# Performance work log

Measured on AMD Instinct MI355X. Metric: run time of the kernel, lower is better.

## Reference

```python
import jax, jax.numpy as jnp
import numpy as np

N = 50000      # nodes
E = 800000     # edges (before self-loops)
IN = 128       # in_channels
C = 64         # hidden_channels (per head)
H = 2          # heads
OUT = 40       # out_channels (classes)
SLOPE = 0.2    # PyG GATConv leaky_relu negative_slope


def setup_inputs() -> dict:
    key = jax.random.key(0)
    ks = jax.random.split(key, 12)
    def glorot(k, shape, fan):
        return (jax.random.normal(k, shape, jnp.float32) / np.float32(np.sqrt(fan)))
    x = jax.random.normal(ks[0], (N, IN), jnp.float32)
    edge_index = jax.random.randint(ks[1], (2, E), 0, N, dtype=jnp.int32)
    return {
        "x": x,
        "edge_index": edge_index,
        "W0": glorot(ks[2], (IN, H * C), IN),
        "a_src0": glorot(ks[3], (H, C), C),
        "a_dst0": glorot(ks[4], (H, C), C),
        "b0": jnp.zeros((H * C,), jnp.float32),
        "W1": glorot(ks[5], (H * C, H * C), H * C),
        "a_src1": glorot(ks[6], (H, C), C),
        "a_dst1": glorot(ks[7], (H, C), C),
        "b1": jnp.zeros((H * C,), jnp.float32),
        "lin_w": glorot(ks[8], (H * C * 2, OUT), H * C * 2),
        "lin_b": jnp.zeros((OUT,), jnp.float32),
    }


def gat_conv(x, W, a_src, a_dst, b, src, dst):
    # x: [N, F_in] -> h: [N, H, C]
    h = (x @ W).reshape(-1, H, C)
    # per-node attention logits (PyG splits a into src/dst halves)
    es = jnp.einsum("nhc,hc->nh", h, a_src)  # [N, H]
    ed = jnp.einsum("nhc,hc->nh", h, a_dst)  # [N, H]
    e = jax.nn.leaky_relu(es[src] + ed[dst], SLOPE)  # [Etot, H]
    # segment softmax over incoming edges of each destination node
    m = jax.ops.segment_max(e, dst, num_segments=N)          # [N, H]
    m = jnp.where(jnp.isneginf(m), 0.0, m)
    w = jnp.exp(e - m[dst])                                  # [Etot, H]
    denom = jax.ops.segment_sum(w, dst, num_segments=N)      # [N, H]
    alpha = w / jnp.maximum(denom[dst], 1e-16)               # [Etot, H]
    # scatter-aggregate messages: [Etot, H, C] -> [N, H, C]
    out = jax.ops.segment_sum(alpha[:, :, None] * h[src], dst, num_segments=N)
    return out.reshape(-1, H * C) + b  # concat=True over heads


def reference(x, edge_index, W0, a_src0, a_dst0, b0, W1, a_src1, a_dst1, b1, lin_w, lin_b):
    # PyG GATConv adds self-loops by default
    loops = jnp.arange(N, dtype=edge_index.dtype)
    src = jnp.concatenate([edge_index[0], loops])
    dst = jnp.concatenate([edge_index[1], loops])
    h1 = jax.nn.elu(gat_conv(x, W0, a_src0, a_dst0, b0, src, dst))   # [N, H*C]
    h2 = jax.nn.elu(gat_conv(h1, W1, a_src1, a_dst1, b1, src, dst))  # [N, H*C]
    h_cat = jnp.concatenate([h1, h2], axis=1)                        # [N, 2*H*C]
    logits = h_cat @ lin_w + lin_b                                   # [N, OUT]
    return jax.nn.log_softmax(logits, axis=1)
```

## Files before the change

### kernel.cpp

```cpp
#include <hip/hip_runtime.h>
#include <hip/hip_fp16.h>
#include <math.h>

#define NN 50000
#define E0 800000
#define ET 850000
#define NBK 196
#define TILE 4096
#define NTILES 208
#define CAP 8192

typedef unsigned int uint32;
typedef unsigned short u16;
typedef __attribute__((ext_vector_type(8))) _Float16 f16x8;
typedef __attribute__((ext_vector_type(4))) float f32x4;

__device__ __forceinline__ u16 f2h(float f) {
  return __half_as_ushort(__float2half(f));
}
__device__ __forceinline__ float h2f(u16 u) {
  return __half2float(__ushort_as_half(u));
}

__global__ __launch_bounds__(256) void partition_prep_kernel(
    const int* __restrict__ ei, int* __restrict__ gcursor, uint32* __restrict__ packed,
    const float* __restrict__ W0, const float* __restrict__ W1,
    const float* __restrict__ lw,
    u16* __restrict__ w0t, u16* __restrict__ w1t, u16* __restrict__ lwt)
{
  __shared__ __align__(16) char smem[23872];
  const int b = blockIdx.x;
  const int tid = threadIdx.x;
  if (b < NTILES) {
    int* hist = (int*)smem;
    int* s    = (int*)(smem + 784);
    int* scanb = (int*)(smem + 1808);
    int* gofs  = (int*)(smem + 2592);
    uint32* shuf = (uint32*)(smem + 3376);
    unsigned char* sbkt = (unsigned char*)(smem + 19760);
    const int t0 = b * TILE;
    for (int i = tid; i < NBK; i += 256) hist[i] = 0;
    __syncthreads();
    int myb[16]; int myr[16]; uint32 mypk[16];
#pragma unroll
    for (int it = 0; it < 4; ++it) {
      const int q = it * 256 + tid;
      const int e4 = t0 + q * 4;
      const bool valid = (e4 < ET);
      int sa[4], da[4];
      if (valid) {
        if (e4 + 3 < E0) {
          int4 sv = *(const int4*)&ei[e4];
          int4 dv = *(const int4*)&ei[E0 + e4];
          sa[0] = sv.x; sa[1] = sv.y; sa[2] = sv.z; sa[3] = sv.w;
          da[0] = dv.x; da[1] = dv.y; da[2] = dv.z; da[3] = dv.w;
        } else {
#pragma unroll
          for (int u = 0; u < 4; ++u) { sa[u] = e4 - E0 + u; da[u] = sa[u]; }
        }
      }
#pragma unroll
      for (int u = 0; u < 4; ++u) {
        const int i = it * 4 + u;
        myb[i] = -1;
        if (valid) {
          const int src = sa[u], dst = da[u];
          myb[i] = dst >> 8;
          mypk[i] = ((uint32)(dst & 255) << 16) | (uint32)src;
          myr[i] = atomicAdd(&hist[myb[i]], 1);
        }
      }
    }
    __syncthreads();
    int v = (tid < NBK) ? hist[tid] : 0;
    int val = v;
    s[tid] = val;
    __syncthreads();
#pragma unroll
    for (int off = 1; off < 256; off <<= 1) {
      int t = (tid >= off) ? s[tid - off] : 0;
      __syncthreads();
      val += t;
      s[tid] = val;
      __syncthreads();
    }
    if (tid < NBK) {
      scanb[tid] = val - v;
      gofs[tid] = (v > 0) ? atomicAdd(&gcursor[tid], v) : 0;
    }
    __syncthreads();
#pragma unroll
    for (int i = 0; i < 16; ++i) {
      if (myb[i] >= 0) {
        int slot = scanb[myb[i]] + myr[i];
        shuf[slot] = mypk[i];
        sbkt[slot] = (unsigned char)myb[i];
      }
    }
    __syncthreads();
    const int tcount = (t0 + TILE <= ET) ? TILE : (ET - t0);
    for (int i = tid; i < tcount; i += 256) {
      int bb = sbkt[i];
      packed[(size_t)bb * CAP + gofs[bb] + (i - scanb[bb])] = shuf[i];
    }
  } else if (b < NTILES + 2) {
    const float* W = (b == NTILES) ? W0 : W1;
    u16* Wt = (b == NTILES) ? w0t : w1t;
    float (*tile)[129] = (float(*)[129])smem;
    for (int k0 = 0; k0 < 128; k0 += 32) {
      __syncthreads();
#pragma unroll
      for (int it = 0; it < 4; ++it) {
        int q = tid + it * 256;
        int kk = q >> 5, n4 = (q & 31) * 4;
        float4 v = *(const float4*)&W[(k0 + kk) * 128 + n4];
        tile[kk][n4 + 0] = v.x; tile[kk][n4 + 1] = v.y;
        tile[kk][n4 + 2] = v.z; tile[kk][n4 + 3] = v.w;
      }
      __syncthreads();
      int n = tid >> 1, h = (tid & 1) * 16;
      __align__(16) u16 tmp[16];
#pragma unroll
      for (int j = 0; j < 16; ++j) tmp[j] = f2h(tile[h + j][n]);
      *(uint4*)&Wt[n * 128 + k0 + h] = *(uint4*)&tmp[0];
      *(uint4*)&Wt[n * 128 + k0 + h + 8] = *(uint4*)&tmp[8];
    }
  } else {
    for (int idx = tid; idx < 48 * 256; idx += 256) {
      int j = idx >> 8, k = idx & 255;
      lwt[idx] = (j < 40) ? f2h(lw[k * 40 + j]) : (u16)0;
    }
  }
}

__device__ __forceinline__ void build_body(
    char* smem, int b,
    const uint32* __restrict__ packed, const int* __restrict__ gcursor,
    int2* __restrict__ rowinfo, u16* __restrict__ csr_src)
{
  int* h      = (int*)smem;
  int* s      = (int*)(smem + 1024);
  int* sc     = (int*)(smem + 2048);
  int* cur    = (int*)(smem + 3072);
  int* ptot_p = (int*)(smem + 4096);
  u16* simg   = (u16*)(smem + 4112);
  const int tid = threadIdx.x;
  const int cnt = gcursor[b];
  const uint32* pk = packed + (size_t)b * CAP;
  h[tid] = 0;
  cur[tid] = 0;
  __syncthreads();
  for (int i = tid; i < cnt; i += 256) atomicAdd(&h[(pk[i] >> 16) & 255], 1);
  __syncthreads();
  const int pd = (h[tid] + 7) & ~7;
  int val = pd;
  s[tid] = val;
  __syncthreads();
#pragma unroll
  for (int off = 1; off < 256; off <<= 1) {
    int t = (tid >= off) ? s[tid - off] : 0;
    __syncthreads();
    val += t;
    s[tid] = val;
    __syncthreads();
  }
  sc[tid] = val - pd;
  if (tid == 255) *ptot_p = val;
  __syncthreads();
  const int ptot = *ptot_p;
  for (int i = tid; i < ptot; i += 256) simg[i] = (u16)NN;
  __syncthreads();
  for (int i = tid; i < cnt; i += 256) {
    uint32 p = pk[i];
    int dl = (p >> 16) & 255;
    int r = atomicAdd(&cur[dl], 1);
    simg[sc[dl] + r] = (u16)(p & 0xFFFFu);
  }
  __syncthreads();
  int n = b * 256 + tid;
  if (n < NN) rowinfo[n] = make_int2(b * CAP + sc[tid], pd);
  uint32* dst = (uint32*)(csr_src + (size_t)b * CAP);
  const uint32* sim32 = (const uint32*)simg;
  for (int i = tid; i < (ptot >> 1); i += 256) dst[i] = sim32[i];
}

__global__ __launch_bounds__(256) void gemm_att_kernel(
    const float* __restrict__ Xf, const u16* __restrict__ Xh,
    const u16* __restrict__ Wt,
    const float* __restrict__ avs, const float* __restrict__ avd,
    u16* __restrict__ hfeat, float* __restrict__ es, float* __restrict__ ed,
    int nnodes,
    const uint32* __restrict__ packed, const int* __restrict__ gcursor,
    int2* __restrict__ rowinfo, u16* __restrict__ csr_src)
{
  __shared__ __align__(16) char smem[20608];
  const int ngemm = (nnodes + 63) >> 6;
  if ((int)blockIdx.x >= ngemm) {
    build_body(smem, (int)blockIdx.x - ngemm, packed, gcursor, rowinfo, csr_src);
    return;
  }
  u16* hout   = (u16*)smem;
  float* es_s = (float*)(smem + 17408);
  float* ed_s = (float*)(smem + 17920);
  const int tid = threadIdx.x;
  const int wid = tid >> 6, lane = tid & 63;
  const int quad = lane >> 4, lc = lane & 15;
  const int n0 = blockIdx.x * 64;
  if (blockIdx.x == 0 && tid < 2) es[2 * NN + tid] = -1e30f;

  const int arow = wid * 16 + lc;
  const int rrow = min(n0 + arow, nnodes - 1);

  f32x4 acc[8];
#pragma unroll
  for (int t = 0; t < 8; ++t) acc[t] = (f32x4){0.f, 0.f, 0.f, 0.f};
#pragma unroll
  for (int ks = 0; ks < 4; ++ks) {
    const int k0 = ks * 32 + quad * 8;
    f16x8 a;
    if (Xf) {
      const float4* xr = (const float4*)&Xf[(size_t)rrow * 128 + k0];
      float4 v0 = xr[0], v1 = xr[1];
      a[0] = (_Float16)v0.x; a[1] = (_Float16)v0.y;
      a[2] = (_Float16)v0.z; a[3] = (_Float16)v0.w;
      a[4] = (_Float16)v1.x; a[5] = (_Float16)v1.y;
      a[6] = (_Float16)v1.z; a[7] = (_Float16)v1.w;
    } else {
      a = *(const f16x8*)&Xh[(size_t)rrow * 128 + k0];
    }
#pragma unroll
    for (int t = 0; t < 8; ++t) {
      f16x8 bfr = *(const f16x8*)&Wt[(t * 16 + lc) * 128 + k0];
      acc[t] = __builtin_amdgcn_mfma_f32_16x16x32_f16(a, bfr, acc[t], 0, 0, 0);
    }
  }

  float av_s[8], av_d[8];
#pragma unroll
  for (int t = 0; t < 8; ++t) { av_s[t] = avs[t * 16 + lc]; av_d[t] = avd[t * 16 + lc]; }
#pragma unroll
  for (int r = 0; r < 4; ++r) {
    float s0 = 0.f, s1 = 0.f, d0 = 0.f, d1 = 0.f;
#pragma unroll
    for (int t = 0; t < 4; ++t) { s0 += acc[t][r] * av_s[t]; d0 += acc[t][r] * av_d[t]; }
#pragma unroll
    for (int t = 4; t < 8; ++t) { s1 += acc[t][r] * av_s[t]; d1 += acc[t][r] * av_d[t]; }
#pragma unroll
    for (int m = 1; m < 16; m <<= 1) {
      s0 += __shfl_xor(s0, m); s1 += __shfl_xor(s1, m);
      d0 += __shfl_xor(d0, m); d1 += __shfl_xor(d1, m);
    }
    if (lc == 0) {
      int row = wid * 16 + quad * 4 + r;
      es_s[row] = s0; es_s[64 + row] = s1;
      ed_s[row] = d0; ed_s[64 + row] = d1;
    }
  }
#pragma unroll
  for (int t = 0; t < 8; ++t)
#pragma unroll
    for (int r = 0; r < 4; ++r)
      hout[(wid * 16 + quad * 4 + r) * 136 + t * 16 + lc] = f2h(acc[t][r]);
  __syncthreads();
#pragma unroll
  for (int it = 0; it < 4; ++it) {
    int g = tid + it * 256;
    int r = g >> 4, c8 = (g & 15) * 8;
    if (n0 + r < nnodes)
      *(uint4*)&hfeat[(size_t)(n0 + r) * 128 + c8] = *(const uint4*)&hout[r * 136 + c8];
  }
  if (tid < 64) {
    int n = n0 + tid;
    if (n < nnodes) {
      es[n * 2 + 0] = es_s[tid];      es[n * 2 + 1] = es_s[64 + tid];
      ed[n * 2 + 0] = ed_s[tid];      ed[n * 2 + 1] = ed_s[64 + tid];
    }
  }
}

__global__ __launch_bounds__(256) void aggregate_kernel(
    const uint4* __restrict__ hfeat4, const float* __restrict__ es, const float* __restrict__ ed,
    const int2* __restrict__ rowinfo, const u16* __restrict__ csr_src,
    const float* __restrict__ bias, u16* __restrict__ out, int nnodes)
{
  int n = (blockIdx.x * blockDim.x + threadIdx.x) >> 6;
  int lane = threadIdx.x & 63;
  if (n >= nnodes) return;
  const int eg = lane >> 4;
  const int fl = lane & 15;
  const int hd = (fl >= 8) ? 1 : 0;
  const int2 ri = rowinfo[n];
  const int nch = ri.y >> 3;
  const int j0 = ri.x + eg;
  const float edn = ed[n * 2 + hd];

  float acc[8];
#pragma unroll
  for (int t = 0; t < 8; ++t) acc[t] = 0.f;
  float den = 0.f;

  int iA0 = csr_src[j0], iA1 = csr_src[j0 + 4];
  float e0 = es[iA0 * 2 + hd] + edn; e0 = fmaxf(e0, 0.2f * e0);
  float e1 = es[iA1 * 2 + hd] + edn; e1 = fmaxf(e1, 0.2f * e1);
  float wA0 = __expf(e0), wA1 = __expf(e1);
  uint4 hA0 = hfeat4[(size_t)iA0 * 16 + fl];
  uint4 hA1 = hfeat4[(size_t)iA1 * 16 + fl];

  for (int c = 0;;) {
    const bool more = (c + 1 < nch);
    float wB0 = 0.f, wB1 = 0.f; uint4 hB0, hB1;
    if (more) {
      const int jb = j0 + (c + 1) * 8;
      int iB0 = csr_src[jb], iB1 = csr_src[jb + 4];
      float f0 = es[iB0 * 2 + hd] + edn; f0 = fmaxf(f0, 0.2f * f0);
      float f1 = es[iB1 * 2 + hd] + edn; f1 = fmaxf(f1, 0.2f * f1);
      wB0 = __expf(f0); wB1 = __expf(f1);
      hB0 = hfeat4[(size_t)iB0 * 16 + fl];
      hB1 = hfeat4[(size_t)iB1 * 16 + fl];
    }
    acc[0] = fmaf(wA0, h2f((u16)(hA0.x & 0xFFFFu)), acc[0]);
    acc[1] = fmaf(wA0, h2f((u16)(hA0.x >> 16)),     acc[1]);
    acc[2] = fmaf(wA0, h2f((u16)(hA0.y & 0xFFFFu)), acc[2]);
    acc[3] = fmaf(wA0, h2f((u16)(hA0.y >> 16)),     acc[3]);
    acc[4] = fmaf(wA0, h2f((u16)(hA0.z & 0xFFFFu)), acc[4]);
    acc[5] = fmaf(wA0, h2f((u16)(hA0.z >> 16)),     acc[5]);
    acc[6] = fmaf(wA0, h2f((u16)(hA0.w & 0xFFFFu)), acc[6]);
    acc[7] = fmaf(wA0, h2f((u16)(hA0.w >> 16)),     acc[7]);
    acc[0] = fmaf(wA1, h2f((u16)(hA1.x & 0xFFFFu)), acc[0]);
    acc[1] = fmaf(wA1, h2f((u16)(hA1.x >> 16)),     acc[1]);
    acc[2] = fmaf(wA1, h2f((u16)(hA1.y & 0xFFFFu)), acc[2]);
    acc[3] = fmaf(wA1, h2f((u16)(hA1.y >> 16)),     acc[3]);
    acc[4] = fmaf(wA1, h2f((u16)(hA1.z & 0xFFFFu)), acc[4]);
    acc[5] = fmaf(wA1, h2f((u16)(hA1.z >> 16)),     acc[5]);
    acc[6] = fmaf(wA1, h2f((u16)(hA1.w & 0xFFFFu)), acc[6]);
    acc[7] = fmaf(wA1, h2f((u16)(hA1.w >> 16)),     acc[7]);
    den += wA0 + wA1;
    if (!more) break;
    wA0 = wB0; wA1 = wB1; hA0 = hB0; hA1 = hB1;
    ++c;
  }

#pragma unroll
  for (int t = 0; t < 8; ++t) {
    acc[t] += __shfl_xor(acc[t], 16);
    acc[t] += __shfl_xor(acc[t], 32);
  }
  den += __shfl_xor(den, 16);
  den += __shfl_xor(den, 32);

  if (eg == 0) {
    float inv = 1.f / den;
    float4 b0 = *(const float4*)&bias[fl * 8];
    float4 b1 = *(const float4*)&bias[fl * 8 + 4];
    float bv[8] = {b0.x, b0.y, b0.z, b0.w, b1.x, b1.y, b1.z, b1.w};
    u16 pk[8];
#pragma unroll
    for (int t = 0; t < 8; ++t) {
      float v = acc[t] * inv + bv[t];
      v = (v > 0.f) ? v : (__expf(v) - 1.f);
      pk[t] = f2h(v);
    }
    uint4 o;
    o.x = (uint32)pk[0] | ((uint32)pk[1] << 16);
    o.y = (uint32)pk[2] | ((uint32)pk[3] << 16);
    o.z = (uint32)pk[4] | ((uint32)pk[5] << 16);
    o.w = (uint32)pk[6] | ((uint32)pk[7] << 16);
    ((uint4*)out)[(size_t)n * 16 + fl] = o;
  }
}

__global__ __launch_bounds__(256) void final_kernel(
    const u16* __restrict__ h1b, const u16* __restrict__ h2b,
    const u16* __restrict__ lwt, const float* __restrict__ lb,
    float* __restrict__ out, int nnodes)
{
  const int tid = threadIdx.x;
  const int wid = tid >> 6, lane = tid & 63;
  const int quad = lane >> 4, lc = lane & 15;
  const int n0 = blockIdx.x * 64;
  const int arow = wid * 16 + lc;
  const int rrow = min(n0 + arow, nnodes - 1);

  f32x4 acc[3];
#pragma unroll
  for (int t = 0; t < 3; ++t) acc[t] = (f32x4){0.f, 0.f, 0.f, 0.f};
#pragma unroll
  for (int ks = 0; ks < 8; ++ks) {
    const u16* hsrc = (ks < 4) ? h1b : h2b;
    const int k0 = (ks & 3) * 32 + quad * 8;
    const int kl = ks * 32 + quad * 8;
    f16x8 a = *(const f16x8*)&hsrc[(size_t)rrow * 128 + k0];
#pragma unroll
    for (int t = 0; t < 3; ++t) {
      f16x8 b = *(const f16x8*)&lwt[(t * 16 + lc) * 256 + kl];
      acc[t] = __builtin_amdgcn_mfma_f32_16x16x32_f16(a, b, acc[t], 0, 0, 0);
    }
  }

  float bv[3];
  bool valid[3];
#pragma unroll
  for (int t = 0; t < 3; ++t) {
    int col = t * 16 + lc;
    valid[t] = (col < 40);
    bv[t] = valid[t] ? lb[col] : 0.f;
  }
#pragma unroll
  for (int r = 0; r < 4; ++r) {
    int row = wid * 16 + quad * 4 + r;
    int n = n0 + row;
    float v[3];
    float mx = -INFINITY;
#pragma unroll
    for (int t = 0; t < 3; ++t) {
      v[t] = acc[t][r] + bv[t];
      if (valid[t]) mx = fmaxf(mx, v[t]);
    }
    mx = fmaxf(mx, __shfl_xor(mx, 1));
    mx = fmaxf(mx, __shfl_xor(mx, 2));
    mx = fmaxf(mx, __shfl_xor(mx, 4));
    mx = fmaxf(mx, __shfl_xor(mx, 8));
    float s = 0.f;
#pragma unroll
    for (int t = 0; t < 3; ++t) if (valid[t]) s += __expf(v[t] - mx);
    s += __shfl_xor(s, 1);
    s += __shfl_xor(s, 2);
    s += __shfl_xor(s, 4);
    s += __shfl_xor(s, 8);
    float lg = mx + __logf(s);
    if (n < nnodes) {
#pragma unroll
      for (int t = 0; t < 3; ++t)
        if (valid[t]) out[(size_t)n * 40 + t * 16 + lc] = v[t] - lg;
    }
  }
}


extern "C" void kernel_launch(void* const* d_in, const int* in_sizes, int n_in,
                              void* d_out, int out_size, void* d_ws, size_t ws_size,
                              hipStream_t stream) {
  const float* x   = (const float*)d_in[0];
  const int*   ei  = (const int*)d_in[1];
  const float* W0  = (const float*)d_in[2];
  const float* as0 = (const float*)d_in[3];
  const float* ad0 = (const float*)d_in[4];
  const float* b0  = (const float*)d_in[5];
  const float* W1  = (const float*)d_in[6];
  const float* as1 = (const float*)d_in[7];
  const float* ad1 = (const float*)d_in[8];
  const float* b1  = (const float*)d_in[9];
  const float* lw  = (const float*)d_in[10];
  const float* lb  = (const float*)d_in[11];
  float* out = (float*)d_out;

  char* p = (char*)d_ws;
  auto carve = [&](size_t bytes) { char* r = p; p += (bytes + 255) & ~(size_t)255; return r; };
  u16* w0t    = (u16*)carve(128 * 128 * 2);
  u16* w1t    = (u16*)carve(128 * 128 * 2);
  u16* lwt    = (u16*)carve(48 * 256 * 2);
  u16* hfeat  = (u16*)carve((size_t)(NN + 1) * 128 * 2);
  u16* h1b    = (u16*)carve((size_t)NN * 128 * 2);
  u16* h2b    = (u16*)carve((size_t)NN * 128 * 2);
  float* es   = (float*)carve((size_t)(NN + 1) * 2 * 4);
  float* ed   = (float*)carve((size_t)NN * 2 * 4);
  int2* rowinfo = (int2*)carve((size_t)NN * 8);
  u16* csr    = (u16*)carve((size_t)NBK * CAP * 2);
  uint32* packed = (uint32*)carve((size_t)NBK * CAP * 4);
  int* gcursor = (int*)carve(NBK * 4);

  hipMemsetAsync(gcursor, 0, NBK * 4, stream);

  const int NG = (NN + 63) / 64;

  partition_prep_kernel<<<NTILES + 3, 256, 0, stream>>>(
      ei, gcursor, packed, W0, W1, lw, w0t, w1t, lwt);

  gemm_att_kernel<<<NG + NBK, 256, 0, stream>>>(
      x, nullptr, w0t, as0, ad0, hfeat, es, ed, NN, packed, gcursor, rowinfo, csr);
  aggregate_kernel<<<(NN * 64 + 255) / 256, 256, 0, stream>>>(
      (const uint4*)hfeat, es, ed, rowinfo, csr, b0, h1b, NN);

  gemm_att_kernel<<<NG, 256, 0, stream>>>(
      nullptr, h1b, w1t, as1, ad1, hfeat, es, ed, NN, packed, gcursor, rowinfo, csr);
  aggregate_kernel<<<(NN * 64 + 255) / 256, 256, 0, stream>>>(
      (const uint4*)hfeat, es, ed, rowinfo, csr, b1, h2b, NN);

  final_kernel<<<NG, 256, 0, stream>>>(h1b, h2b, lwt, lb, out, NN);
}
```

Before: 234.6 us.

## Halve partition tile size, use wave-shuffle block scan, make aggregation grid-stride

Partition tiles shrink from 4096 to 2048 edges, doubling the tile block count and cutting shared memory per block. The Hillis-Steele shared-memory scans in the partition and CSR-build bodies become a wave shuffle scan plus a 4-wave fixup, removing most barriers. The aggregate kernel becomes a persistent grid-stride loop over nodes with 2048 blocks and the bias loaded once per wave. Risks include more global atomics on the bucket cursors and load imbalance in the fixed-grid aggregation.

Result: no change. 238.7 us (+1.8%).

```diff
diff --git a/kernel.cpp b/kernel.cpp
--- a/kernel.cpp
+++ b/kernel.cpp
@@ -6,8 +6,8 @@
 #define E0 800000
 #define ET 850000
 #define NBK 196
-#define TILE 4096
-#define NTILES 208
+#define TILE 2048
+#define NTILES 416
 #define CAP 8192
 
 typedef unsigned int uint32;
@@ -20,6 +20,22 @@
 }
 __device__ __forceinline__ float h2f(u16 u) {
   return __half2float(__ushort_as_half(u));
+}
+
+__device__ __forceinline__ int block_incl_scan(int v, int tid, int* wsum) {
+  const int lane = tid & 63, wid = tid >> 6;
+  int val = v;
+#pragma unroll
+  for (int off = 1; off < 64; off <<= 1) {
+    int t = __shfl_up(val, off);
+    if (lane >= off) val += t;
+  }
+  if (lane == 63) wsum[wid] = val;
+  __syncthreads();
+  int wofs = 0;
+#pragma unroll
+  for (int w = 0; w < 4; ++w) wofs += (w < wid) ? wsum[w] : 0;
+  return val + wofs;
 }
 
 __global__ __launch_bounds__(256) void partition_prep_kernel(
@@ -28,22 +44,22 @@
     const float* __restrict__ lw,
     u16* __restrict__ w0t, u16* __restrict__ w1t, u16* __restrict__ lwt)
 {
-  __shared__ __align__(16) char smem[23872];
+  __shared__ __align__(16) char smem[16512];
   const int b = blockIdx.x;
   const int tid = threadIdx.x;
   if (b < NTILES) {
-    int* hist = (int*)smem;
-    int* s    = (int*)(smem + 784);
-    int* scanb = (int*)(smem + 1808);
-    int* gofs  = (int*)(smem + 2592);
-    uint32* shuf = (uint32*)(smem + 3376);
-    unsigned char* sbkt = (unsigned char*)(smem + 19760);
+    int* hist  = (int*)smem;
+    int* scanb = (int*)(smem + 1024);
+    int* gofs  = (int*)(smem + 2048);
+    int* wsum  = (int*)(smem + 3072);
+    uint32* shuf = (uint32*)(smem + 3088);
+    unsigned char* sbkt = (unsigned char*)(smem + 11280);
     const int t0 = b * TILE;
-    for (int i = tid; i < NBK; i += 256) hist[i] = 0;
+    hist[tid] = 0;
     __syncthreads();
-    int myb[16]; int myr[16]; uint32 mypk[16];
-#pragma unroll
-    for (int it = 0; it < 4; ++it) {
+    int myb[8]; int myr[8]; uint32 mypk[8];
+#pragma unroll
+    for (int it = 0; it < 2; ++it) {
       const int q = it * 256 + tid;
       const int e4 = t0 + q * 4;
       const bool valid = (e4 < ET);
@@ -72,25 +88,15 @@
       }
     }
     __syncthreads();
-    int v = (tid < NBK) ? hist[tid] : 0;
-    int val = v;
-    s[tid] = val;
+    const int v = (tid < NBK) ? hist[tid] : 0;
+    const int incl = block_incl_scan(v, tid, wsum);
+    if (tid < NBK) {
+      scanb[tid] = incl - v;
+      gofs[tid] = (v > 0) ? atomicAdd(&gcursor[tid], v) : 0;
+    }
     __syncthreads();
 #pragma unroll
-    for (int off = 1; off < 256; off <<= 1) {
-      int t = (tid >= off) ? s[tid - off] : 0;
-      __syncthreads();
-      val += t;
-      s[tid] = val;
-      __syncthreads();
-    }
-    if (tid < NBK) {
-      scanb[tid] = val - v;
-      gofs[tid] = (v > 0) ? atomicAdd(&gcursor[tid], v) : 0;
-    }
-    __syncthreads();
-#pragma unroll
-    for (int i = 0; i < 16; ++i) {
+    for (int i = 0; i < 8; ++i) {
       if (myb[i] >= 0) {
         int slot = scanb[myb[i]] + myr[i];
         shuf[slot] = mypk[i];
@@ -139,11 +145,11 @@
     int2* __restrict__ rowinfo, u16* __restrict__ csr_src)
 {
   int* h      = (int*)smem;
-  int* s      = (int*)(smem + 1024);
-  int* sc     = (int*)(smem + 2048);
-  int* cur    = (int*)(smem + 3072);
-  int* ptot_p = (int*)(smem + 4096);
-  u16* simg   = (u16*)(smem + 4112);
+  int* sc     = (int*)(smem + 1024);
+  int* cur    = (int*)(smem + 2048);
+  int* wsum   = (int*)(smem + 3072);
+  int* ptot_p = (int*)(smem + 3088);
+  u16* simg   = (u16*)(smem + 3104);
   const int tid = threadIdx.x;
   const int cnt = gcursor[b];
   const uint32* pk = packed + (size_t)b * CAP;
@@ -153,19 +159,9 @@
   for (int i = tid; i < cnt; i += 256) atomicAdd(&h[(pk[i] >> 16) & 255], 1);
   __syncthreads();
   const int pd = (h[tid] + 7) & ~7;
-  int val = pd;
-  s[tid] = val;
-  __syncthreads();
-#pragma unroll
-  for (int off = 1; off < 256; off <<= 1) {
-    int t = (tid >= off) ? s[tid - off] : 0;
-    __syncthreads();
-    val += t;
-    s[tid] = val;
-    __syncthreads();
-  }
-  sc[tid] = val - pd;
-  if (tid == 255) *ptot_p = val;
+  const int incl = block_incl_scan(pd, tid, wsum);
+  sc[tid] = incl - pd;
+  if (tid == 255) *ptot_p = incl;
   __syncthreads();
   const int ptot = *ptot_p;
   for (int i = tid; i < ptot; i += 256) simg[i] = (u16)NN;
@@ -283,89 +279,97 @@
     const int2* __restrict__ rowinfo, const u16* __restrict__ csr_src,
     const float* __restrict__ bias, u16* __restrict__ out, int nnodes)
 {
-  int n = (blockIdx.x * blockDim.x + threadIdx.x) >> 6;
-  int lane = threadIdx.x & 63;
-  if (n >= nnodes) return;
+  const int wgid = (blockIdx.x * blockDim.x + threadIdx.x) >> 6;
+  const int nwaves = (gridDim.x * blockDim.x) >> 6;
+  const int lane = threadIdx.x & 63;
   const int eg = lane >> 4;
   const int fl = lane & 15;
   const int hd = (fl >= 8) ? 1 : 0;
-  const int2 ri = rowinfo[n];
-  const int nch = ri.y >> 3;
-  const int j0 = ri.x + eg;
-  const float edn = ed[n * 2 + hd];
-
-  float acc[8];
-#pragma unroll
-  for (int t = 0; t < 8; ++t) acc[t] = 0.f;
-  float den = 0.f;
-
-  int iA0 = csr_src[j0], iA1 = csr_src[j0 + 4];
-  float e0 = es[iA0 * 2 + hd] + edn; e0 = fmaxf(e0, 0.2f * e0);
-  float e1 = es[iA1 * 2 + hd] + edn; e1 = fmaxf(e1, 0.2f * e1);
-  float wA0 = __expf(e0), wA1 = __expf(e1);
-  uint4 hA0 = hfeat4[(size_t)iA0 * 16 + fl];
-  uint4 hA1 = hfeat4[(size_t)iA1 * 16 + fl];
-
-  for (int c = 0;;) {
-    const bool more = (c + 1 < nch);
-    float wB0 = 0.f, wB1 = 0.f; uint4 hB0, hB1;
-    if (more) {
-      const int jb = j0 + (c + 1) * 8;
-      int iB0 = csr_src[jb], iB1 = csr_src[jb + 4];
-      float f0 = es[iB0 * 2 + hd] + edn; f0 = fmaxf(f0, 0.2f * f0);
-      float f1 = es[iB1 * 2 + hd] + edn; f1 = fmaxf(f1, 0.2f * f1);
-      wB0 = __expf(f0); wB1 = __expf(f1);
-      hB0 = hfeat4[(size_t)iB0 * 16 + fl];
-      hB1 = hfeat4[(size_t)iB1 * 16 + fl];
-    }
-    acc[0] = fmaf(wA0, h2f((u16)(hA0.x & 0xFFFFu)), acc[0]);
-    acc[1] = fmaf(wA0, h2f((u16)(hA0.x >> 16)),     acc[1]);
-    acc[2] = fmaf(wA0, h2f((u16)(hA0.y & 0xFFFFu)), acc[2]);
-    acc[3] = fmaf(wA0, h2f((u16)(hA0.y >> 16)),     acc[3]);
-    acc[4] = fmaf(wA0, h2f((u16)(hA0.z & 0xFFFFu)), acc[4]);
-    acc[5] = fmaf(wA0, h2f((u16)(hA0.z >> 16)),     acc[5]);
-    acc[6] = fmaf(wA0, h2f((u16)(hA0.w & 0xFFFFu)), acc[6]);
-    acc[7] = fmaf(wA0, h2f((u16)(hA0.w >> 16)),     acc[7]);
-    acc[0] = fmaf(wA1, h2f((u16)(hA1.x & 0xFFFFu)), acc[0]);
-    acc[1] = fmaf(wA1, h2f((u16)(hA1.x >> 16)),     acc[1]);
-    acc[2] = fmaf(wA1, h2f((u16)(hA1.y & 0xFFFFu)), acc[2]);
-    acc[3] = fmaf(wA1, h2f((u16)(hA1.y >> 16)),     acc[3]);
-    acc[4] = fmaf(wA1, h2f((u16)(hA1.z & 0xFFFFu)), acc[4]);
-    acc[5] = fmaf(wA1, h2f((u16)(hA1.z >> 16)),     acc[5]);
-    acc[6] = fmaf(wA1, h2f((u16)(hA1.w & 0xFFFFu)), acc[6]);
-    acc[7] = fmaf(wA1, h2f((u16)(hA1.w >> 16)),     acc[7]);
-    den += wA0 + wA1;
-    if (!more) break;
-    wA0 = wB0; wA1 = wB1; hA0 = hB0; hA1 = hB1;
-    ++c;
-  }
-
-#pragma unroll
-  for (int t = 0; t < 8; ++t) {
-    acc[t] += __shfl_xor(acc[t], 16);
-    acc[t] += __shfl_xor(acc[t], 32);
-  }
-  den += __shfl_xor(den, 16);
-  den += __shfl_xor(den, 32);
-
-  if (eg == 0) {
-    float inv = 1.f / den;
+
+  float bv[8];
+  {
     float4 b0 = *(const float4*)&bias[fl * 8];
     float4 b1 = *(const float4*)&bias[fl * 8 + 4];
-    float bv[8] = {b0.x, b0.y, b0.z, b0.w, b1.x, b1.y, b1.z, b1.w};
-    u16 pk[8];
+    bv[0] = b0.x; bv[1] = b0.y; bv[2] = b0.z; bv[3] = b0.w;
+    bv[4] = b1.x; bv[5] = b1.y; bv[6] = b1.z; bv[7] = b1.w;
+  }
+
+  for (int n = wgid; n < nnodes; n += nwaves) {
+    const int2 ri = rowinfo[n];
+    const int nch = ri.y >> 3;
+    const int j0 = ri.x + eg;
+    const float edn = ed[n * 2 + hd];
+
+    float acc[8];
+#pragma unroll
+    for (int t = 0; t < 8; ++t) acc[t] = 0.f;
+    float den = 0.f;
+
+    int iA0 = csr_src[j0], iA1 = csr_src[j0 + 4];
+    float e0 = es[iA0 * 2 + hd] + edn; e0 = fmaxf(e0, 0.2f * e0);
+    float e1 = es[iA1 * 2 + hd] + edn; e1 = fmaxf(e1, 0.2f * e1);
+    float wA0 = __expf(e0), wA1 = __expf(e1);
+    uint4 hA0 = hfeat4[(size_t)iA0 * 16 + fl];
+    uint4 hA1 = hfeat4[(size_t)iA1 * 16 + fl];
+
+    for (int c = 0;;) {
+      const bool more = (c + 1 < nch);
+      float wB0 = 0.f, wB1 = 0.f; uint4 hB0, hB1;
+      if (more) {
+        const int jb = j0 + (c + 1) * 8;
+        int iB0 = csr_src[jb], iB1 = csr_src[jb + 4];
+        float f0 = es[iB0 * 2 + hd] + edn; f0 = fmaxf(f0, 0.2f * f0);
+        float f1 = es[iB1 * 2 + hd] + edn; f1 = fmaxf(f1, 0.2f * f1);
+        wB0 = __expf(f0); wB1 = __expf(f1);
+        hB0 = hfeat4[(size_t)iB0 * 16 + fl];
+        hB1 = hfeat4[(size_t)iB1 * 16 + fl];
+      }
+      acc[0] = fmaf(wA0, h2f((u16)(hA0.x & 0xFFFFu)), acc[0]);
+      acc[1] = fmaf(wA0, h2f((u16)(hA0.x >> 16)),     acc[1]);
+      acc[2] = fmaf(wA0, h2f((u16)(hA0.y & 0xFFFFu)), acc[2]);
+      acc[3] = fmaf(wA0, h2f((u16)(hA0.y >> 16)),     acc[3]);
+      acc[4] = fmaf(wA0, h2f((u16)(hA0.z & 0xFFFFu)), acc[4]);
+      acc[5] = fmaf(wA0, h2f((u16)(hA0.z >> 16)),     acc[5]);
+      acc[6] = fmaf(wA0, h2f((u16)(hA0.w & 0xFFFFu)), acc[6]);
+      acc[7] = fmaf(wA0, h2f((u16)(hA0.w >> 16)),     acc[7]);
+      acc[0] = fmaf(wA1, h2f((u16)(hA1.x & 0xFFFFu)), acc[0]);
+      acc[1] = fmaf(wA1, h2f((u16)(hA1.x >> 16)),     acc[1]);
+      acc[2] = fmaf(wA1, h2f((u16)(hA1.y & 0xFFFFu)), acc[2]);
+      acc[3] = fmaf(wA1, h2f((u16)(hA1.y >> 16)),     acc[3]);
+      acc[4] = fmaf(wA1, h2f((u16)(hA1.z & 0xFFFFu)), acc[4]);
+      acc[5] = fmaf(wA1, h2f((u16)(hA1.z >> 16)),     acc[5]);
+      acc[6] = fmaf(wA1, h2f((u16)(hA1.w & 0xFFFFu)), acc[6]);
+      acc[7] = fmaf(wA1, h2f((u16)(hA1.w >> 16)),     acc[7]);
+      den += wA0 + wA1;
+      if (!more) break;
+      wA0 = wB0; wA1 = wB1; hA0 = hB0; hA1 = hB1;
+      ++c;
+    }
+
 #pragma unroll
     for (int t = 0; t < 8; ++t) {
-      float v = acc[t] * inv + bv[t];
-      v = (v > 0.f) ? v : (__expf(v) - 1.f);
-      pk[t] = f2h(v);
-    }
-    uint4 o;
-    o.x = (uint32)pk[0] | ((uint32)pk[1] << 16);
-    o.y = (uint32)pk[2] | ((uint32)pk[3] << 16);
-    o.z = (uint32)pk[4] | ((uint32)pk[5] << 16);
-    o.w = (uint32)pk[6] | ((uint32)pk[7] << 16);
-    ((uint4*)out)[(size_t)n * 16 + fl] = o;
+      acc[t] += __shfl_xor(acc[t], 16);
+      acc[t] += __shfl_xor(acc[t], 32);
+    }
+    den += __shfl_xor(den, 16);
+    den += __shfl_xor(den, 32);
+
+    if (eg == 0) {
+      float inv = 1.f / den;
+      u16 pk[8];
+#pragma unroll
+      for (int t = 0; t < 8; ++t) {
+        float v = acc[t] * inv + bv[t];
+        v = (v > 0.f) ? v : (__expf(v) - 1.f);
+        pk[t] = f2h(v);
+      }
+      uint4 o;
+      o.x = (uint32)pk[0] | ((uint32)pk[1] << 16);
+      o.y = (uint32)pk[2] | ((uint32)pk[3] << 16);
+      o.z = (uint32)pk[4] | ((uint32)pk[5] << 16);
+      o.w = (uint32)pk[6] | ((uint32)pk[7] << 16);
+      ((uint4*)out)[(size_t)n * 16 + fl] = o;
+    }
   }
 }
 
@@ -472,18 +476,19 @@
   hipMemsetAsync(gcursor, 0, NBK * 4, stream);
 
   const int NG = (NN + 63) / 64;
+  const int AGG_BLOCKS = 2048;
 
   partition_prep_kernel<<<NTILES + 3, 256, 0, stream>>>(
       ei, gcursor, packed, W0, W1, lw, w0t, w1t, lwt);
 
   gemm_att_kernel<<<NG + NBK, 256, 0, stream>>>(
       x, nullptr, w0t, as0, ad0, hfeat, es, ed, NN, packed, gcursor, rowinfo, csr);
-  aggregate_kernel<<<(NN * 64 + 255) / 256, 256, 0, stream>>>(
+  aggregate_kernel<<<AGG_BLOCKS, 256, 0, stream>>>(
       (const uint4*)hfeat, es, ed, rowinfo, csr, b0, h1b, NN);
 
   gemm_att_kernel<<<NG, 256, 0, stream>>>(
       nullptr, h1b, w1t, as1, ad1, hfeat, es, ed, NN, packed, gcursor, rowinfo, csr);
-  aggregate_kernel<<<(NN * 64 + 255) / 256, 256, 0, stream>>>(
+  aggregate_kernel<<<AGG_BLOCKS, 256, 0, stream>>>(
       (const uint4*)hfeat, es, ed, rowinfo, csr, b1, h2b, NN);
 
   final_kernel<<<NG, 256, 0, stream>>>(h1b, h2b, lwt, lb, out, NN);
```
